# Performance work log

Hardware: AMD Instinct MI355X
Metric: run time of the kernel (lower is better)

The kernel has to match this reference:

```python
import jax, jax.numpy as jnp
import numpy as np

N = 2048      # num_nodes
B = 64        # batch
D_IN = 2      # input_dim per node
UNITS = 64    # hidden dim
K = 2         # max_diffusion_step
N_SUP = 2     # dual_random_walk -> two supports
M = N_SUP * K + 1           # num_matrices = 5
IN_SIZE = D_IN + UNITS      # 66
E = 65536                   # nnz per support


def setup_inputs() -> dict:
    key = jax.random.key(0)
    ks = jax.random.split(key, 10)
    inputs = jax.random.normal(ks[0], (B, N * D_IN), jnp.float32)
    state = jax.random.normal(ks[1], (B, N * UNITS), jnp.float32)
    edges1 = jax.random.randint(ks[2], (2, E), 0, N)
    vals1 = jax.random.uniform(ks[3], (E,), jnp.float32) / 32.0  # ~row-stochastic scale
    edges2 = jax.random.randint(ks[4], (2, E), 0, N)
    vals2 = jax.random.uniform(ks[5], (E,), jnp.float32) / 32.0
    W_gate = jax.random.normal(ks[6], (IN_SIZE * M, 2 * UNITS), jnp.float32) * 0.08
    b_gate = jnp.ones((2 * UNITS,), jnp.float32)  # bias_start=1.0 for gate
    W_cand = jax.random.normal(ks[7], (IN_SIZE * M, UNITS), jnp.float32) * 0.08
    b_cand = jnp.zeros((UNITS,), jnp.float32)
    return dict(inputs=inputs, state=state, edges1=edges1, vals1=vals1,
                edges2=edges2, vals2=vals2, W_gate=W_gate, b_gate=b_gate,
                W_cand=W_cand, b_cand=b_cand)


def _spmm(rows, cols, vals, x):
    # sparse [N,N] @ dense [N,F] via gather + segment_sum
    return jax.ops.segment_sum(x[cols] * vals[:, None], rows, num_segments=N)


def _dconv(inp, st, supports, W, b, out_dim):
    # inputs/state -> [B, N, F] concat, F = IN_SIZE
    x = jnp.concatenate([inp.reshape(B, N, -1), st.reshape(B, N, -1)], axis=2)
    f = x.shape[2]
    x0 = x.transpose(1, 2, 0).reshape(N, f * B)  # [N, F*B]
    xs = [x0]
    for (rows, cols, vals) in supports:
        x1 = _spmm(rows, cols, vals, x0)
        xs.append(x1)
        xk_1, xk_2 = x1, x0
        for _ in range(2, K + 1):  # Chebyshev recursion: x_k = 2 S x_{k-1} - x_{k-2}
            xk = 2.0 * _spmm(rows, cols, vals, xk_1) - xk_2
            xs.append(xk)
            xk_1, xk_2 = xk, xk_1
    xcat = jnp.stack(xs, 0).reshape(M, N, f, B)
    xcat = xcat.transpose(3, 1, 2, 0).reshape(B * N, f * M)  # [B*N, F*M]
    out = xcat @ W + b
    return out.reshape(B, N * out_dim)


def reference(inputs, state, edges1, vals1, edges2, vals2, W_gate, b_gate, W_cand, b_cand):
    supports = [(edges1[0], edges1[1], vals1), (edges2[0], edges2[1], vals2)]
    value = jax.nn.sigmoid(_dconv(inputs, state, supports, W_gate, b_gate, 2 * UNITS))
    value = value.reshape(B, N, 2 * UNITS)
    r = value[:, :, :UNITS].reshape(B, N * UNITS)
    u = value[:, :, UNITS:].reshape(B, N * UNITS)
    c = jnp.tanh(_dconv(inputs, r * state, supports, W_cand, b_cand, UNITS))
    new_state = u * state + (1.0 - u) * c
    return new_state
```

## Files before the change

### kernel.cpp

```cpp
#include <hip/hip_runtime.h>
#include <stdint.h>

#define NN 2048
#define BB 64
#define EE 65536
#define APITCH 360
#define XSN ((size_t)NN*4096)
#define XIN ((size_t)NN*128)

typedef unsigned short u16;
typedef __bf16 bf16x8 __attribute__((ext_vector_type(8)));
typedef float f32x4 __attribute__((ext_vector_type(4)));
typedef float f32x2 __attribute__((ext_vector_type(2)));

__device__ __forceinline__ float bf2f(u16 h){ return __uint_as_float(((unsigned)h)<<16); }
__device__ __forceinline__ u16 f2bf(float f){
  unsigned u = __float_as_uint(f);
  u += 0x7fffu + ((u>>16)&1u);
  return (u16)(u>>16);
}
__device__ __forceinline__ float loadf(const void* p, size_t i, int bfflag){
  return bfflag ? bf2f(((const u16*)p)[i]) : ((const float*)p)[i];
}
__device__ __forceinline__ f32x2 up2(unsigned u){
  f32x2 r; r.x = __uint_as_float(u<<16); r.y = __uint_as_float(u & 0xffff0000u); return r;
}
__device__ __forceinline__ unsigned pk2(f32x2 t){
  return (unsigned)f2bf(t.x) | ((unsigned)f2bf(t.y)<<16);
}
__device__ __forceinline__ void accv(float v, uint4 d, f32x2* a){
  f32x2 vv = {v, v};
  a[0] += vv*up2(d.x); a[1] += vv*up2(d.y);
  a[2] += vv*up2(d.z); a[3] += vv*up2(d.w);
}

__global__ void probe_k(const unsigned* __restrict__ vals, int* __restrict__ flag){
  int cnt = 0;
  for (int i=0;i<64;i++){
    unsigned lo = vals[i] & 0xffffu;
    if (lo >= 0x2800u && lo < 0x3D80u) cnt++;
  }
  *flag = (cnt >= 32) ? 1 : 0;
}

__global__ void hist2_k(const int* __restrict__ e1, const int* __restrict__ e2,
                        int* __restrict__ cnt){
  int b = blockIdx.x;
  if (b < 256) atomicAdd(&cnt[e1[b*256 + threadIdx.x]], 1);
  else atomicAdd(&cnt[2048 + e2[(b-256)*256 + threadIdx.x]], 1);
}

__global__ void scan2_k(const int* __restrict__ cntA, int* __restrict__ rpA, int* __restrict__ curA){
  __shared__ int s[1024];
  const int* cnt = cntA + blockIdx.x*2048;
  int* rp  = rpA  + blockIdx.x*2049;
  int* cur = curA + blockIdx.x*2048;
  int t = threadIdx.x;
  int c0 = cnt[2*t], c1 = cnt[2*t+1];
  int ps = c0 + c1;
  s[t] = ps;
  __syncthreads();
  for (int off=1; off<1024; off<<=1){
    int v = (t>=off) ? s[t-off] : 0;
    __syncthreads();
    s[t] += v;
    __syncthreads();
  }
  int excl = s[t] - ps;
  rp[2*t] = excl;  cur[2*t] = excl;
  rp[2*t+1] = excl + c0;  cur[2*t+1] = excl + c0;
  if (t==0) rp[2048] = EE;
}

__global__ void scatter2_k(const int* __restrict__ e1, const void* __restrict__ v1,
                           const int* __restrict__ e2, const void* __restrict__ v2,
                           int* __restrict__ curA, int2* __restrict__ scvA,
                           const int* __restrict__ flag){
  int bfflag = *flag;
  int b = blockIdx.x;
  const int* rows; const int* cols; const void* vals; int* cur; int2* scv; int e;
  if (b < 256){ rows=e1; cols=e1+EE; vals=v1; cur=curA; scv=scvA; e=b*256+threadIdx.x; }
  else { rows=e2; cols=e2+EE; vals=v2; cur=curA+2048; scv=scvA+EE; e=(b-256)*256+threadIdx.x; }
  int r = rows[e];
  int p = atomicAdd(&cur[r], 1);
  int2 cv; cv.x = cols[e]; cv.y = __float_as_int(loadf(vals, e, bfflag));
  scv[p] = cv;
}

__global__ void pack2_k(const void* __restrict__ Wg, const void* __restrict__ Wc,
                        u16* __restrict__ Wfg, u16* __restrict__ Wfc,
                        const int* __restrict__ flag){
  int bfflag = *flag;
  int b = blockIdx.x;
  const void* W; u16* Wf; int O, OT, i;
  if (b < 176){ W=Wg; Wf=Wfg; O=128; OT=8; i=b*256+threadIdx.x; }
  else { W=Wc; Wf=Wfc; O=64; OT=4; i=(b-176)*256+threadIdx.x; }
  int j = i & 7, L = (i>>3)&63, tq = i>>9;
  int t = tq % OT, q = tq / OT;
  int o = t*16 + (L&15);
  int kk = q*32 + (L>>4)*8 + j;
  float v = 0.f;
  if (kk < 330){ int m = kk/66, f = kk - m*66; v = loadf(W, (size_t)(f*5+m)*O + o, bfflag); }
  Wf[i] = f2bf(v);
}

__global__ void build_x0_k(const void* __restrict__ inp, const void* __restrict__ st,
                           u16* __restrict__ XSb, u16* __restrict__ XIb,
                           const int* __restrict__ flag){
  int bfflag = *flag, n = blockIdx.x, tid = threadIdx.x;
  if (bfflag){
    const uint4* sp = (const uint4*)st;
    uint4* xp = (uint4*)(XSb + (size_t)n*4096);
    #pragma unroll
    for (int it=0; it<2; ++it){
      int r = tid + it*256;
      int b = r>>3, v4 = r&7;
      xp[r] = sp[(size_t)b*(NN*8) + (size_t)n*8 + v4];
    }
    if (tid < 64){
      ((unsigned*)XIb)[n*64 + tid] = ((const unsigned*)inp)[(size_t)tid*NN + n];
    }
  } else {
    for (int i=tid; i<4096; i+=256){
      int b=i>>6, f=i&63;
      XSb[(size_t)n*4096+i] = f2bf(((const float*)st)[(size_t)b*(NN*64) + n*64 + f]);
    }
    for (int i=tid; i<128; i+=256){
      int b=i>>1, f=i&1;
      XIb[(size_t)n*128+i] = f2bf(((const float*)inp)[(size_t)b*(NN*2) + n*2 + f]);
    }
  }
}

template<int CHEB>
__global__ __launch_bounds__(64) void spmm_k(
    u16* __restrict__ XSb, u16* __restrict__ XIb,
    const int* __restrict__ rpA, const int2* __restrict__ scvA){
  int sup = blockIdx.y;
  const int* rp = rpA + sup*2049;
  const int2* scv = scvA + sup*EE;
  const int srcm = CHEB ? (sup?3:1) : 0;
  const int dstm = CHEB ? (sup?4:2) : (sup?3:1);
  int tid = threadIdx.x;
  int bx = blockIdx.x;
  if (bx < NN*8){
    int ch = bx & 7, n = bx >> 3;
    int e0 = rp[n], e1 = rp[n+1];
    const uint4* src = (const uint4*)(XSb + srcm*XSN);
    int off = ch*64 + tid;
    f32x2 a[4] = {{0.f,0.f},{0.f,0.f},{0.f,0.f},{0.f,0.f}};
    int e = e0;
    for (; e+3 < e1; e += 4){
      int2 c0=scv[e], c1=scv[e+1], c2=scv[e+2], c3=scv[e+3];
      uint4 d0 = src[((size_t)c0.x<<9) + off];
      uint4 d1 = src[((size_t)c1.x<<9) + off];
      uint4 d2 = src[((size_t)c2.x<<9) + off];
      uint4 d3 = src[((size_t)c3.x<<9) + off];
      accv(__int_as_float(c0.y), d0, a);
      accv(__int_as_float(c1.y), d1, a);
      accv(__int_as_float(c2.y), d2, a);
      accv(__int_as_float(c3.y), d3, a);
    }
    for (; e < e1; ++e){
      int2 c0 = scv[e];
      accv(__int_as_float(c0.y), src[((size_t)c0.x<<9) + off], a);
    }
    uint4* dst = (uint4*)(XSb + dstm*XSN);
    uint4 w;
    if (CHEB){
      uint4 o = ((const uint4*)XSb)[((size_t)n<<9) + off];
      f32x2 t;
      t = 2.f*a[0] - up2(o.x); w.x = pk2(t);
      t = 2.f*a[1] - up2(o.y); w.y = pk2(t);
      t = 2.f*a[2] - up2(o.z); w.z = pk2(t);
      t = 2.f*a[3] - up2(o.w); w.w = pk2(t);
    } else {
      w.x = pk2(a[0]); w.y = pk2(a[1]); w.z = pk2(a[2]); w.w = pk2(a[3]);
    }
    dst[((size_t)n<<9) + off] = w;
  } else {
    int idx = bx - NN*8;
    int n = idx*2 + (tid>>5), m = tid & 31;
    int e0 = rp[n], e1 = rp[n+1];
    const uint2* src = (const uint2*)(XIb + srcm*XIN);
    f32x2 a0 = {0.f,0.f}, a1 = {0.f,0.f};
    for (int e=e0; e<e1; ++e){
      int2 cv = scv[e];
      uint2 d = src[cv.x*32 + m];
      f32x2 vv = {__int_as_float(cv.y), __int_as_float(cv.y)};
      a0 += vv*up2(d.x); a1 += vv*up2(d.y);
    }
    uint2* dst = (uint2*)(XIb + dstm*XIN);
    if (CHEB){
      uint2 o = ((const uint2*)XIb)[n*32 + m];
      a0 = 2.f*a0 - up2(o.x); a1 = 2.f*a1 - up2(o.y);
    }
    uint2 w; w.x = pk2(a0); w.y = pk2(a1);
    dst[n*32 + m] = w;
  }
}

template<int OT, int MODE>
__global__ __launch_bounds__(256) void gemm_k(
    u16* __restrict__ XSb, const u16* __restrict__ XIb,
    const u16* __restrict__ Wf, const void* __restrict__ bias,
    const void* __restrict__ state, void* __restrict__ outp,
    const int* __restrict__ flag){
  __shared__ __align__(16) u16 A[64*APITCH];
  unsigned* A32 = (unsigned*)A;
  int tid = threadIdx.x, n = blockIdx.x;
  int bfflag = *flag;
  #pragma unroll
  for (int m=0;m<5;m++){
    const uint4* src = (const uint4*)(XSb + (size_t)m*XSN + ((size_t)n<<12));
    #pragma unroll
    for (int it=0; it<2; ++it){
      int r = tid + it*256;
      uint4 d = src[r];
      int b = r>>3, f0 = (r&7)*8;
      int o2 = (b*APITCH + m*66 + 2 + f0) >> 1;
      A32[o2+0]=d.x; A32[o2+1]=d.y; A32[o2+2]=d.z; A32[o2+3]=d.w;
    }
  }
  for (int i=tid; i<320; i+=256){
    int m = i>>6, b = i&63;
    unsigned v = ((const unsigned*)(XIb + (size_t)m*XIN))[n*64 + b];
    A32[(b*APITCH + m*66)>>1] = v;
  }
  for (int i=tid; i<64*11; i+=256){
    int b = i/11, j = i - b*11;
    A32[((b*APITCH + 330)>>1) + j] = 0;
  }
  __syncthreads();
  int lane = tid & 63, w = tid >> 6;
  int m16 = lane & 15, q4 = lane >> 4;
  f32x4 acc[OT];
  #pragma unroll
  for (int t=0;t<OT;t++) acc[t] = (f32x4){0.f,0.f,0.f,0.f};
  const u16* arow = A + (w*16 + m16)*APITCH + q4*8;
  const bf16x8* wp = (const bf16x8*)Wf;
  #pragma unroll
  for (int q=0;q<11;q++){
    bf16x8 af = *((const bf16x8*)(arow + q*32));
    #pragma unroll
    for (int t=0;t<OT;t++){
      bf16x8 bfr = wp[(q*OT+t)*64 + lane];
      acc[t] = __builtin_amdgcn_mfma_f32_16x16x32_bf16(af, bfr, acc[t], 0, 0, 0);
    }
  }
  #pragma unroll
  for (int t=0;t<OT;t++){
    int o = t*16 + m16;
    float bo = loadf(bias, o, bfflag);
    #pragma unroll
    for (int r=0;r<4;r++){
      int b = w*16 + q4*4 + r;
      float x = acc[t][r] + bo;
      if (MODE==0){
        float s = 1.f/(1.f + __expf(-x));
        if (o < 64){
          float st = loadf(state, (size_t)b*(NN*64) + n*64 + o, bfflag);
          XSb[((size_t)n<<12) + b*64 + o] = f2bf(s*st);
        } else {
          size_t idx = (size_t)b*(NN*64) + n*64 + (o-64);
          if (bfflag) ((u16*)outp)[idx] = f2bf(s); else ((float*)outp)[idx] = s;
        }
      } else {
        float c = tanhf(x);
        size_t idx = (size_t)b*(NN*64) + n*64 + o;
        float uu = bfflag ? bf2f(((const u16*)outp)[idx]) : ((const float*)outp)[idx];
        float st = loadf(state, idx, bfflag);
        float ns = uu*st + (1.f-uu)*c;
        if (bfflag) ((u16*)outp)[idx] = f2bf(ns); else ((float*)outp)[idx] = ns;
      }
    }
  }
}

extern "C" void kernel_launch(void* const* d_in, const int* in_sizes, int n_in,
                              void* d_out, int out_size, void* d_ws, size_t ws_size,
                              hipStream_t stream) {
  const void* inputs = d_in[0];
  const void* state  = d_in[1];
  const int* edges1 = (const int*)d_in[2];
  const void* vals1  = d_in[3];
  const int* edges2 = (const int*)d_in[4];
  const void* vals2  = d_in[5];
  const void* Wg     = d_in[6];
  const void* bg     = d_in[7];
  const void* Wc     = d_in[8];
  const void* bc     = d_in[9];

  char* ws = (char*)d_ws;
  size_t off = 0;
  auto get = [&](size_t bytes)->void*{
    void* p = ws + off; off = (off + bytes + 255) & ~(size_t)255; return p;
  };
  u16* XSb = (u16*)get(5*XSN*2);
  u16* XIb = (u16*)get(5*XIN*2);
  u16* Wfg = (u16*)get(11*8*64*8*2);
  u16* Wfc = (u16*)get(11*4*64*8*2);
  int* cnt  = (int*)get(2*2048*4);
  int* rp   = (int*)get(2*2049*4);
  int* cur  = (int*)get(2*2048*4);
  int* flag = (int*)get(4);
  int2* scv = (int2*)get((size_t)2*EE*8);

  probe_k<<<1,1,0,stream>>>((const unsigned*)vals1, flag);
  hipMemsetAsync(cnt, 0, 2*2048*4, stream);
  hist2_k<<<512,256,0,stream>>>(edges1, edges2, cnt);
  scan2_k<<<2,1024,0,stream>>>(cnt, rp, cur);
  scatter2_k<<<512,256,0,stream>>>(edges1, vals1, edges2, vals2, cur, scv, flag);
  pack2_k<<<264,256,0,stream>>>(Wg, Wc, Wfg, Wfc, flag);
  build_x0_k<<<NN,256,0,stream>>>(inputs, state, XSb, XIb, flag);

  dim3 sg(NN*8 + NN/2, 2);
  spmm_k<0><<<sg,64,0,stream>>>(XSb, XIb, rp, scv);
  spmm_k<1><<<sg,64,0,stream>>>(XSb, XIb, rp, scv);
  gemm_k<8,0><<<NN,256,0,stream>>>(XSb, XIb, Wfg, bg, state, d_out, flag);
  spmm_k<0><<<sg,64,0,stream>>>(XSb, XIb, rp, scv);
  spmm_k<1><<<sg,64,0,stream>>>(XSb, XIb, rp, scv);
  gemm_k<4,1><<<NN,256,0,stream>>>(XSb, XIb, Wfc, bc, state, d_out, flag);
}
```

Baseline: 474.0 us.

## Keep GEMM weight fragments in registers and load A fragments directly from global

The GEMM kernels no longer stage the concatenated activation tile in LDS. Each single-wave block now holds the full weight fragments in registers and loops over 8 row tiles, loading A fragments straight from global memory. The K ordering is repacked so the 64-wide state features come first and the 2 input features are packed at the end, which keeps fragment loads aligned. The candidate GEMM also double-buffers its A fragments. This removes the LDS staging and barrier and reuses weights across tiles, at the cost of heavy register pressure (up to 88 weight vectors) and less parallelism from 1024 one-wave blocks.

```diff
diff --git a/kernel.cpp b/kernel.cpp
--- a/kernel.cpp
+++ b/kernel.cpp
@@ -2,9 +2,7 @@
 #include <stdint.h>
 
 #define NN 2048
-#define BB 64
 #define EE 65536
-#define APITCH 360
 #define XSN ((size_t)NN*4096)
 #define XIN ((size_t)NN*128)
 
@@ -100,7 +98,8 @@
   int o = t*16 + (L&15);
   int kk = q*32 + (L>>4)*8 + j;
   float v = 0.f;
-  if (kk < 330){ int m = kk/66, f = kk - m*66; v = loadf(W, (size_t)(f*5+m)*O + o, bfflag); }
+  if (kk < 320){ int m = kk>>6, f = (kk&63)+2; v = loadf(W, (size_t)(f*5+m)*O + o, bfflag); }
+  else if (kk < 330){ int tt = kk-320; int m = tt>>1, f = tt&1; v = loadf(W, (size_t)(f*5+m)*O + o, bfflag); }
   Wf[i] = f2bf(v);
 }
 
@@ -200,78 +199,97 @@
   }
 }
 
-template<int OT, int MODE>
-__global__ __launch_bounds__(256) void gemm_k(
+__device__ __forceinline__ void load_afrag(bf16x8* af, const u16* __restrict__ XSb,
+                                           const unsigned* __restrict__ XI32,
+                                           int n, int rt4, int m16, int q4){
+  const uint4* xs4 = (const uint4*)XSb;
+  int b = rt4*16 + m16;
+  size_t base = (size_t)n*512 + (size_t)b*8 + q4;
+  #pragma unroll
+  for (int q=0;q<10;q++){
+    union { uint4 v; bf16x8 b; } u;
+    u.v = xs4[(size_t)(q>>1)*(XSN/8) + base + (q&1)*4];
+    af[q] = u.b;
+  }
+  union { unsigned w[4]; bf16x8 b; } t;
+  t.w[0]=0; t.w[1]=0; t.w[2]=0; t.w[3]=0;
+  if (q4==0){
+    #pragma unroll
+    for (int mm=0;mm<4;mm++) t.w[mm] = XI32[mm*(XIN/2) + n*64 + b];
+  } else if (q4==1){
+    t.w[0] = XI32[4*(XIN/2) + n*64 + b];
+  }
+  af[10] = t.b;
+}
+
+template<int OT, int MODE, int R, int DBUF>
+__global__ __launch_bounds__(64,1) void gemm_k(
     u16* __restrict__ XSb, const u16* __restrict__ XIb,
     const u16* __restrict__ Wf, const void* __restrict__ bias,
     const void* __restrict__ state, void* __restrict__ outp,
     const int* __restrict__ flag){
-  __shared__ __align__(16) u16 A[64*APITCH];
-  unsigned* A32 = (unsigned*)A;
-  int tid = threadIdx.x, n = blockIdx.x;
+  int lane = threadIdx.x;
+  int m16 = lane & 15, q4 = lane >> 4;
   int bfflag = *flag;
-  #pragma unroll
-  for (int m=0;m<5;m++){
-    const uint4* src = (const uint4*)(XSb + (size_t)m*XSN + ((size_t)n<<12));
-    #pragma unroll
-    for (int it=0; it<2; ++it){
-      int r = tid + it*256;
-      uint4 d = src[r];
-      int b = r>>3, f0 = (r&7)*8;
-      int o2 = (b*APITCH + m*66 + 2 + f0) >> 1;
-      A32[o2+0]=d.x; A32[o2+1]=d.y; A32[o2+2]=d.z; A32[o2+3]=d.w;
-    }
-  }
-  for (int i=tid; i<320; i+=256){
-    int m = i>>6, b = i&63;
-    unsigned v = ((const unsigned*)(XIb + (size_t)m*XIN))[n*64 + b];
-    A32[(b*APITCH + m*66)>>1] = v;
-  }
-  for (int i=tid; i<64*11; i+=256){
-    int b = i/11, j = i - b*11;
-    A32[((b*APITCH + 330)>>1) + j] = 0;
-  }
-  __syncthreads();
-  int lane = tid & 63, w = tid >> 6;
-  int m16 = lane & 15, q4 = lane >> 4;
-  f32x4 acc[OT];
-  #pragma unroll
-  for (int t=0;t<OT;t++) acc[t] = (f32x4){0.f,0.f,0.f,0.f};
-  const u16* arow = A + (w*16 + m16)*APITCH + q4*8;
   const bf16x8* wp = (const bf16x8*)Wf;
+  bf16x8 wfr[11][OT];
   #pragma unroll
   for (int q=0;q<11;q++){
-    bf16x8 af = *((const bf16x8*)(arow + q*32));
+    #pragma unroll
+    for (int t=0;t<OT;t++) wfr[q][t] = wp[(q*OT+t)*64 + lane];
+  }
+  const unsigned* XI32 = (const unsigned*)XIb;
+  int rt0 = blockIdx.x * R;
+
+  bf16x8 afA[11], afB[11];
+  if (DBUF) load_afrag(afA, XSb, XI32, rt0>>2, rt0&3, m16, q4);
+  #pragma unroll
+  for (int i=0;i<R;i++){
+    int rt = rt0 + i;
+    int n = rt>>2, rt4 = rt&3;
+    bf16x8* af;
+    if (DBUF){
+      af = (i&1) ? afB : afA;
+      bf16x8* afn = (i&1) ? afA : afB;
+      if (i+1 < R) load_afrag(afn, XSb, XI32, (rt+1)>>2, (rt+1)&3, m16, q4);
+    } else {
+      af = afA;
+      load_afrag(afA, XSb, XI32, n, rt4, m16, q4);
+    }
+    f32x4 acc[OT];
+    #pragma unroll
+    for (int t=0;t<OT;t++) acc[t] = (f32x4){0.f,0.f,0.f,0.f};
+    #pragma unroll
+    for (int q=0;q<11;q++){
+      #pragma unroll
+      for (int t=0;t<OT;t++)
+        acc[t] = __builtin_amdgcn_mfma_f32_16x16x32_bf16(af[q], wfr[q][t], acc[t], 0, 0, 0);
+    }
     #pragma unroll
     for (int t=0;t<OT;t++){
-      bf16x8 bfr = wp[(q*OT+t)*64 + lane];
-      acc[t] = __builtin_amdgcn_mfma_f32_16x16x32_bf16(af, bfr, acc[t], 0, 0, 0);
-    }
-  }
-  #pragma unroll
-  for (int t=0;t<OT;t++){
-    int o = t*16 + m16;
-    float bo = loadf(bias, o, bfflag);
-    #pragma unroll
-    for (int r=0;r<4;r++){
-      int b = w*16 + q4*4 + r;
-      float x = acc[t][r] + bo;
-      if (MODE==0){
-        float s = 1.f/(1.f + __expf(-x));
-        if (o < 64){
-          float st = loadf(state, (size_t)b*(NN*64) + n*64 + o, bfflag);
-          XSb[((size_t)n<<12) + b*64 + o] = f2bf(s*st);
+      int o = t*16 + m16;
+      float bo = loadf(bias, o, bfflag);
+      #pragma unroll
+      for (int r=0;r<4;r++){
+        int b = rt4*16 + q4*4 + r;
+        float x = acc[t][r] + bo;
+        if (MODE==0){
+          float s = 1.f/(1.f + __expf(-x));
+          if (t < 4){
+            float st = loadf(state, (size_t)b*(NN*64) + (size_t)n*64 + o, bfflag);
+            XSb[(size_t)n*4096 + b*64 + o] = f2bf(s*st);
+          } else {
+            size_t idx = (size_t)b*(NN*64) + (size_t)n*64 + (o-64);
+            if (bfflag) ((u16*)outp)[idx] = f2bf(s); else ((float*)outp)[idx] = s;
+          }
         } else {
-          size_t idx = (size_t)b*(NN*64) + n*64 + (o-64);
-          if (bfflag) ((u16*)outp)[idx] = f2bf(s); else ((float*)outp)[idx] = s;
+          float c = tanhf(x);
+          size_t idx = (size_t)b*(NN*64) + (size_t)n*64 + o;
+          float uu = bfflag ? bf2f(((const u16*)outp)[idx]) : ((const float*)outp)[idx];
+          float st = loadf(state, idx, bfflag);
+          float ns = uu*st + (1.f-uu)*c;
+          if (bfflag) ((u16*)outp)[idx] = f2bf(ns); else ((float*)outp)[idx] = ns;
         }
-      } else {
-        float c = tanhf(x);
-        size_t idx = (size_t)b*(NN*64) + n*64 + o;
-        float uu = bfflag ? bf2f(((const u16*)outp)[idx]) : ((const float*)outp)[idx];
-        float st = loadf(state, idx, bfflag);
-        float ns = uu*st + (1.f-uu)*c;
-        if (bfflag) ((u16*)outp)[idx] = f2bf(ns); else ((float*)outp)[idx] = ns;
       }
     }
   }
@@ -317,8 +335,8 @@
   dim3 sg(NN*8 + NN/2, 2);
   spmm_k<0><<<sg,64,0,stream>>>(XSb, XIb, rp, scv);
   spmm_k<1><<<sg,64,0,stream>>>(XSb, XIb, rp, scv);
-  gemm_k<8,0><<<NN,256,0,stream>>>(XSb, XIb, Wfg, bg, state, d_out, flag);
+  gemm_k<8,0,8,0><<<1024,64,0,stream>>>(XSb, XIb, Wfg, bg, state, d_out, flag);
   spmm_k<0><<<sg,64,0,stream>>>(XSb, XIb, rp, scv);
   spmm_k<1><<<sg,64,0,stream>>>(XSb, XIb, rp, scv);
-  gemm_k<4,1><<<NN,256,0,stream>>>(XSb, XIb, Wfc, bc, state, d_out, flag);
-}
+  gemm_k<4,1,8,1><<<1024,64,0,stream>>>(XSb, XIb, Wfc, bc, state, d_out, flag);
+}
```

Result: slower. 505.4 us (+6.6%).

## Reorder GEMM K-layout for aligned LDS stores and keep weights in registers

Applied to the files above, without the earlier changes.

The GEMM's shared A tile is repacked so the 64 state features of each diffusion matrix sit at 16-byte-aligned offsets, with the 2 input features moved to the tail. This allows single uint4 LDS stores instead of four scalar ones, and the weight packing is permuted to match. Each wave now preloads its slice of output-column weight fragments into registers once, overlapped with the LDS fill, and loops over four row tiles instead of re-reading all weights from global memory per K-step. The one-thread probe kernel becomes a 64-lane ballot. The cost is higher register pressure from holding 11×TW fragments.

```diff
diff --git a/kernel.cpp b/kernel.cpp
--- a/kernel.cpp
+++ b/kernel.cpp
@@ -2,7 +2,6 @@
 #include <stdint.h>
 
 #define NN 2048
-#define BB 64
 #define EE 65536
 #define APITCH 360
 #define XSN ((size_t)NN*4096)
@@ -35,12 +34,10 @@
 }
 
 __global__ void probe_k(const unsigned* __restrict__ vals, int* __restrict__ flag){
-  int cnt = 0;
-  for (int i=0;i<64;i++){
-    unsigned lo = vals[i] & 0xffffu;
-    if (lo >= 0x2800u && lo < 0x3D80u) cnt++;
-  }
-  *flag = (cnt >= 32) ? 1 : 0;
+  int i = threadIdx.x;
+  unsigned lo = vals[i] & 0xffffu;
+  unsigned long long m = __ballot(lo >= 0x2800u && lo < 0x3D80u);
+  if (i==0) *flag = (__popcll(m) >= 32) ? 1 : 0;
 }
 
 __global__ void hist2_k(const int* __restrict__ e1, const int* __restrict__ e2,
@@ -100,7 +97,8 @@
   int o = t*16 + (L&15);
   int kk = q*32 + (L>>4)*8 + j;
   float v = 0.f;
-  if (kk < 330){ int m = kk/66, f = kk - m*66; v = loadf(W, (size_t)(f*5+m)*O + o, bfflag); }
+  if (kk < 320){ int m = kk>>6, f = (kk&63)+2; v = loadf(W, (size_t)(f*5+m)*O + o, bfflag); }
+  else if (kk < 330){ int tt = kk-320; int m = tt>>1, f = tt&1; v = loadf(W, (size_t)(f*5+m)*O + o, bfflag); }
   Wf[i] = f2bf(v);
 }
 
@@ -207,7 +205,6 @@
     const void* __restrict__ state, void* __restrict__ outp,
     const int* __restrict__ flag){
   __shared__ __align__(16) u16 A[64*APITCH];
-  unsigned* A32 = (unsigned*)A;
   int tid = threadIdx.x, n = blockIdx.x;
   int bfflag = *flag;
   #pragma unroll
@@ -218,60 +215,68 @@
       int r = tid + it*256;
       uint4 d = src[r];
       int b = r>>3, f0 = (r&7)*8;
-      int o2 = (b*APITCH + m*66 + 2 + f0) >> 1;
-      A32[o2+0]=d.x; A32[o2+1]=d.y; A32[o2+2]=d.z; A32[o2+3]=d.w;
+      *(uint4*)&A[b*APITCH + m*64 + f0] = d;
     }
   }
   for (int i=tid; i<320; i+=256){
     int m = i>>6, b = i&63;
-    unsigned v = ((const unsigned*)(XIb + (size_t)m*XIN))[n*64 + b];
-    A32[(b*APITCH + m*66)>>1] = v;
-  }
-  for (int i=tid; i<64*11; i+=256){
-    int b = i/11, j = i - b*11;
-    A32[((b*APITCH + 330)>>1) + j] = 0;
-  }
-  __syncthreads();
+    unsigned v = ((const unsigned*)XIb)[(size_t)m*(XIN/2) + n*64 + b];
+    *(unsigned*)&A[b*APITCH + 320 + 2*m] = v;
+  }
+  for (int i=tid; i<64*15; i+=256){
+    int b = i/15, j = i - b*15;
+    *(unsigned*)&A[b*APITCH + 330 + 2*j] = 0;
+  }
+  const int TW = OT/4;
   int lane = tid & 63, w = tid >> 6;
   int m16 = lane & 15, q4 = lane >> 4;
-  f32x4 acc[OT];
-  #pragma unroll
-  for (int t=0;t<OT;t++) acc[t] = (f32x4){0.f,0.f,0.f,0.f};
-  const u16* arow = A + (w*16 + m16)*APITCH + q4*8;
   const bf16x8* wp = (const bf16x8*)Wf;
+  bf16x8 wfr[11][TW];
   #pragma unroll
   for (int q=0;q<11;q++){
-    bf16x8 af = *((const bf16x8*)(arow + q*32));
-    #pragma unroll
-    for (int t=0;t<OT;t++){
-      bf16x8 bfr = wp[(q*OT+t)*64 + lane];
-      acc[t] = __builtin_amdgcn_mfma_f32_16x16x32_bf16(af, bfr, acc[t], 0, 0, 0);
-    }
-  }
+    #pragma unroll
+    for (int i=0;i<TW;i++) wfr[q][i] = wp[(q*OT + (w + 4*i))*64 + lane];
+  }
+  __syncthreads();
   #pragma unroll
-  for (int t=0;t<OT;t++){
-    int o = t*16 + m16;
-    float bo = loadf(bias, o, bfflag);
-    #pragma unroll
-    for (int r=0;r<4;r++){
-      int b = w*16 + q4*4 + r;
-      float x = acc[t][r] + bo;
-      if (MODE==0){
-        float s = 1.f/(1.f + __expf(-x));
-        if (o < 64){
-          float st = loadf(state, (size_t)b*(NN*64) + n*64 + o, bfflag);
-          XSb[((size_t)n<<12) + b*64 + o] = f2bf(s*st);
+  for (int rt4=0; rt4<4; ++rt4){
+    const u16* arow = A + (rt4*16 + m16)*APITCH + q4*8;
+    f32x4 acc[TW];
+    #pragma unroll
+    for (int i=0;i<TW;i++) acc[i] = (f32x4){0.f,0.f,0.f,0.f};
+    #pragma unroll
+    for (int q=0;q<11;q++){
+      bf16x8 af = *((const bf16x8*)(arow + q*32));
+      #pragma unroll
+      for (int i=0;i<TW;i++)
+        acc[i] = __builtin_amdgcn_mfma_f32_16x16x32_bf16(af, wfr[q][i], acc[i], 0, 0, 0);
+    }
+    #pragma unroll
+    for (int i=0;i<TW;i++){
+      int t = w + 4*i;
+      int o = t*16 + m16;
+      float bo = loadf(bias, o, bfflag);
+      #pragma unroll
+      for (int r=0;r<4;r++){
+        int b = rt4*16 + q4*4 + r;
+        float x = acc[i][r] + bo;
+        if (MODE==0){
+          float s = 1.f/(1.f + __expf(-x));
+          if (i==0){
+            float st = loadf(state, (size_t)b*(NN*64) + (size_t)n*64 + o, bfflag);
+            XSb[((size_t)n<<12) + b*64 + o] = f2bf(s*st);
+          } else {
+            size_t idx = (size_t)b*(NN*64) + (size_t)n*64 + (o-64);
+            if (bfflag) ((u16*)outp)[idx] = f2bf(s); else ((float*)outp)[idx] = s;
+          }
         } else {
-          size_t idx = (size_t)b*(NN*64) + n*64 + (o-64);
-          if (bfflag) ((u16*)outp)[idx] = f2bf(s); else ((float*)outp)[idx] = s;
+          float c = tanhf(x);
+          size_t idx = (size_t)b*(NN*64) + (size_t)n*64 + o;
+          float uu = bfflag ? bf2f(((const u16*)outp)[idx]) : ((const float*)outp)[idx];
+          float st = loadf(state, idx, bfflag);
+          float ns = uu*st + (1.f-uu)*c;
+          if (bfflag) ((u16*)outp)[idx] = f2bf(ns); else ((float*)outp)[idx] = ns;
         }
-      } else {
-        float c = tanhf(x);
-        size_t idx = (size_t)b*(NN*64) + n*64 + o;
-        float uu = bfflag ? bf2f(((const u16*)outp)[idx]) : ((const float*)outp)[idx];
-        float st = loadf(state, idx, bfflag);
-        float ns = uu*st + (1.f-uu)*c;
-        if (bfflag) ((u16*)outp)[idx] = f2bf(ns); else ((float*)outp)[idx] = ns;
       }
     }
   }
@@ -306,7 +311,7 @@
   int* flag = (int*)get(4);
   int2* scv = (int2*)get((size_t)2*EE*8);
 
-  probe_k<<<1,1,0,stream>>>((const unsigned*)vals1, flag);
+  probe_k<<<1,64,0,stream>>>((const unsigned*)vals1, flag);
   hipMemsetAsync(cnt, 0, 2*2048*4, stream);
   hist2_k<<<512,256,0,stream>>>(edges1, edges2, cnt);
   scan2_k<<<2,1024,0,stream>>>(cnt, rp, cur);
```

After: 447.0 us. 1.06x faster.
